# Kernel optimization log

Hardware: AMD Instinct MI355X
Metric: run time of the kernel (lower is better)

The kernel has to match this reference:

```python
import jax, jax.numpy as jnp
import numpy as np

W_IN = 0.001
W_OUT = 1.0
TOL = 1e-8
N_POINTS = 1_048_576


def _octahedron_hull():
    # Palette vertices: +/- unit axes -> convex hull is an octahedron with 8 triangular faces.
    V = np.array([[1, 0, 0], [-1, 0, 0], [0, 1, 0], [0, -1, 0], [0, 0, 1], [0, 0, -1]],
                 dtype=np.float32)
    faces = []
    for sx in (0, 1):
        for sy in (0, 1):
            for sz in (0, 1):
                faces.append([sx, 2 + sy, 4 + sz])
    F = np.array(faces)            # (8,3) vertex indices
    tris = V[F]                    # (8,3,3) triangle vertices
    a, b, c = tris[:, 0], tris[:, 1], tris[:, 2]
    n = np.cross(b - a, c - a)
    n = n / np.linalg.norm(n, axis=-1, keepdims=True)
    flip = np.sum(n * a, -1) < 0   # orient outward (hull centroid is origin)
    n = np.where(flip[:, None], -n, n)
    off = np.sum(n * a, -1)        # face plane offsets: n.x = off on the face
    return V, tris.astype(np.float32), n.astype(np.float32), off.astype(np.float32)


def setup_inputs() -> dict:
    key = jax.random.key(0)
    V, tris, normals, offsets = _octahedron_hull()
    pts = jax.random.normal(key, (N_POINTS, 3), jnp.float32) * 0.35  # mix of inside/outside
    return {
        "inp_points": pts,
        "hull_vertices": jnp.asarray(V),
        "hull_tris": jnp.asarray(tris),
        "face_normals": jnp.asarray(normals),
        "face_offsets": jnp.asarray(offsets),
    }


def _closest_point_on_tris(p, a, b, c):
    # Ericson's closest-point-on-triangle, broadcast over (N,1,3) points x (1,F,3) triangles.
    eps = 1e-20
    ab = b - a
    ac = c - a
    ap = p - a
    d1 = jnp.sum(ab * ap, -1)
    d2 = jnp.sum(ac * ap, -1)
    bp = p - b
    d3 = jnp.sum(ab * bp, -1)
    d4 = jnp.sum(ac * bp, -1)
    cp = p - c
    d5 = jnp.sum(ab * cp, -1)
    d6 = jnp.sum(ac * cp, -1)
    vc = d1 * d4 - d3 * d2
    vb = d5 * d2 - d1 * d6
    va = d3 * d6 - d5 * d4
    # face interior (lowest priority)
    denom = va + vb + vc
    denom = jnp.where(jnp.abs(denom) > eps, denom, 1.0)
    v = (vb / denom)[..., None]
    w = (vc / denom)[..., None]
    res = a + ab * v + ac * w
    # edge BC
    d43 = d4 - d3
    d56 = d5 - d6
    cond = (va <= 0) & (d43 >= 0) & (d56 >= 0)
    t = (d43 / jnp.where(jnp.abs(d43 + d56) > eps, d43 + d56, 1.0))[..., None]
    res = jnp.where(cond[..., None], b + t * (c - b), res)
    # edge AC
    cond = (vb <= 0) & (d2 >= 0) & (d6 <= 0)
    t = (d2 / jnp.where(jnp.abs(d2 - d6) > eps, d2 - d6, 1.0))[..., None]
    res = jnp.where(cond[..., None], a + t * ac, res)
    # edge AB
    cond = (vc <= 0) & (d1 >= 0) & (d3 <= 0)
    t = (d1 / jnp.where(jnp.abs(d1 - d3) > eps, d1 - d3, 1.0))[..., None]
    res = jnp.where(cond[..., None], a + t * ab, res)
    # vertex regions (highest priority)
    res = jnp.where(((d6 >= 0) & (d5 <= d6))[..., None], c, res)
    res = jnp.where(((d3 >= 0) & (d4 <= d3))[..., None], b, res)
    res = jnp.where(((d1 <= 0) & (d2 <= 0))[..., None], a, res)
    return res


def reference(inp_points, hull_vertices, hull_tris, face_normals, face_offsets):
    p = inp_points  # (N,3)
    # find_simplex >= 0  <=>  point inside convex hull: all face half-spaces satisfied
    inside = jnp.all(p @ face_normals.T - face_offsets <= TOL, axis=-1)  # (N,)
    n_in = jnp.sum(inside)
    # knn_points K=1 -> min SQUARED distance to hull vertices, averaged over inside points
    d2v = jnp.min(jnp.sum((p[:, None, :] - hull_vertices[None]) ** 2, -1), axis=-1)  # (N,)
    loss_in = jnp.where(
        n_in > 0,
        W_IN * jnp.sum(jnp.where(inside, d2v, 0.0)) / jnp.maximum(n_in, 1).astype(p.dtype),
        jnp.asarray(0.0, p.dtype),
    )
    # outside points: min point-triangle distance over all hull faces -> closest point (constant)
    a = hull_tris[None, :, 0]  # (1,F,3)
    b = hull_tris[None, :, 1]
    c = hull_tris[None, :, 2]
    cand = _closest_point_on_tris(p[:, None, :], a, b, c)        # (N,F,3)
    d2 = jnp.sum((p[:, None, :] - cand) ** 2, -1)                # (N,F)
    idx = jnp.argmin(d2, axis=-1)
    closest = jnp.take_along_axis(cand, idx[:, None, None], axis=1)[:, 0, :]  # (N,3)
    closest = jax.lax.stop_gradient(closest)  # torch computes this path in detached numpy
    sq = jnp.sum((p - closest) ** 2, -1)      # per-point sum-of-squares (mse 'none' .sum(-1))
    outside = ~inside
    n_out = jnp.sum(outside)
    loss_out = jnp.where(
        n_out > 0,
        W_OUT * jnp.max(jnp.where(outside, sq, 0.0)),
        jnp.asarray(0.0, p.dtype),
    )
    return loss_in + loss_out
```

## Files before the change

kernel.cpp:

```cpp
#include <hip/hip_runtime.h>

#define NP 1048576
#define BLOCK 256
#define PPT 4
#define NBLK (NP / (BLOCK * PPT))
#define GROUPS 32
#define GSIZE (NBLK / GROUPS)
#define W_IN 0.001f
#define W_OUT 1.0f
#define TOL 1e-8f
#define SQRT3 1.7320508f

__device__ __forceinline__ void drain_vmem() {
    asm volatile("s_waitcnt vmcnt(0)" ::: "memory");
}


__global__ __launch_bounds__(BLOCK) void pbl_fused(
    const float* __restrict__ pts, float* __restrict__ ws, float* __restrict__ out)
{
    __shared__ float s_s[BLOCK/64], s_c[BLOCK/64], s_m[BLOCK/64];
    __shared__ int s_last;

    const int lt = threadIdx.x;
    const int tid = blockIdx.x * BLOCK + lt;
    const float4* p4 = (const float4*)pts;
    float4 f0 = p4[tid*3+0];
    float4 f1 = p4[tid*3+1];
    float4 f2 = p4[tid*3+2];
    float px[PPT] = {f0.x, f0.w, f1.z, f2.y};
    float py[PPT] = {f0.y, f1.x, f1.w, f2.z};
    float pz[PPT] = {f0.z, f1.y, f2.x, f2.w};

    float sum_in = 0.f, cnt_in = 0.f, mx_out = 0.f;
    #pragma unroll
    for (int i = 0; i < PPT; ++i) {
        float ux = fabsf(px[i]), uy = fabsf(py[i]), uz = fabsf(pz[i]);
        float s1 = ux + uy + uz;
        float hi = fmaxf(ux, fmaxf(uy, uz));
        float lo = fminf(ux, fminf(uy, uz));
        float mid = s1 - hi - lo;
        float ss = fmaf(px[i], px[i], fmaf(py[i], py[i], pz[i]*pz[i]));

        bool inside = (s1 - 1.f) <= TOL * SQRT3;
        float d2v = fmaf(-2.f, hi, ss) + 1.f;

        float t3 = (s1 - 1.f) * (1.f/3.f);
        float t2 = (hi + mid - 1.f) * 0.5f;
        float t1 = hi - 1.f;
        float d2_3 = 3.f * t3 * t3;
        float d2_2 = fmaf(lo, lo, 2.f * t2 * t2);
        float d2_1 = fmaf(t1, t1, fmaf(mid, mid, lo * lo));
        float sq = (lo > t3) ? d2_3 : ((mid > t2) ? d2_2 : d2_1);

        sum_in += inside ? d2v : 0.f;
        cnt_in += inside ? 1.f : 0.f;
        mx_out  = inside ? mx_out : fmaxf(mx_out, sq);
    }

    #pragma unroll
    for (int o = 32; o > 0; o >>= 1) {
        sum_in += __shfl_down(sum_in, o);
        cnt_in += __shfl_down(cnt_in, o);
        mx_out  = fmaxf(mx_out, __shfl_down(mx_out, o));
    }
    const int wave = lt >> 6;
    if ((lt & 63) == 0) { s_s[wave] = sum_in; s_c[wave] = cnt_in; s_m[wave] = mx_out; }
    __syncthreads();

    unsigned* wsu = (unsigned*)ws;
    const int g = blockIdx.x & (GROUPS - 1);

    if (lt == 0) {
        float S = 0.f, C = 0.f, M = 0.f;
        #pragma unroll
        for (int i = 0; i < BLOCK/64; ++i) { S += s_s[i]; C += s_c[i]; M = fmaxf(M, s_m[i]); }
        __hip_atomic_store(&ws[blockIdx.x],          S, __ATOMIC_RELAXED, __HIP_MEMORY_SCOPE_AGENT);
        __hip_atomic_store(&ws[NBLK + blockIdx.x],   C, __ATOMIC_RELAXED, __HIP_MEMORY_SCOPE_AGENT);
        __hip_atomic_store(&ws[2*NBLK + blockIdx.x], M, __ATOMIC_RELAXED, __HIP_MEMORY_SCOPE_AGENT);
        drain_vmem();
        unsigned ret = __hip_atomic_fetch_add(&wsu[3*NBLK + (g << 4)], 1u,
                                              __ATOMIC_RELAXED, __HIP_MEMORY_SCOPE_AGENT);
        s_last = ((ret & (GSIZE - 1)) == (GSIZE - 1)) ? 1 : 0;
    }
    __syncthreads();

    if (s_last && lt < 64) {
        const int lane = lt;
        float S = 0.f, C = 0.f, M = 0.f;
        if (lane < GSIZE) {
            int b = g + (lane << 5);
            S = __hip_atomic_load(&ws[b],          __ATOMIC_RELAXED, __HIP_MEMORY_SCOPE_AGENT);
            C = __hip_atomic_load(&ws[NBLK + b],   __ATOMIC_RELAXED, __HIP_MEMORY_SCOPE_AGENT);
            M = __hip_atomic_load(&ws[2*NBLK + b], __ATOMIC_RELAXED, __HIP_MEMORY_SCOPE_AGENT);
        }
        #pragma unroll
        for (int o = 32; o > 0; o >>= 1) {
            S += __shfl_down(S, o);
            C += __shfl_down(C, o);
            M  = fmaxf(M, __shfl_down(M, o));
        }
        int last2 = 0;
        if (lane == 0) {
            __hip_atomic_store(&ws[3584 + g], S, __ATOMIC_RELAXED, __HIP_MEMORY_SCOPE_AGENT);
            __hip_atomic_store(&ws[3616 + g], C, __ATOMIC_RELAXED, __HIP_MEMORY_SCOPE_AGENT);
            __hip_atomic_store(&ws[3648 + g], M, __ATOMIC_RELAXED, __HIP_MEMORY_SCOPE_AGENT);
            drain_vmem();
            unsigned r2 = __hip_atomic_fetch_add(&wsu[3712], 1u,
                                                 __ATOMIC_RELAXED, __HIP_MEMORY_SCOPE_AGENT);
            last2 = ((r2 & (GROUPS - 1)) == (GROUPS - 1)) ? 1 : 0;
        }
        last2 = __shfl(last2, 0);
        if (last2) {
            float S2 = 0.f, C2 = 0.f, M2 = 0.f;
            if (lane < GROUPS) {
                S2 = __hip_atomic_load(&ws[3584 + lane], __ATOMIC_RELAXED, __HIP_MEMORY_SCOPE_AGENT);
                C2 = __hip_atomic_load(&ws[3616 + lane], __ATOMIC_RELAXED, __HIP_MEMORY_SCOPE_AGENT);
                M2 = __hip_atomic_load(&ws[3648 + lane], __ATOMIC_RELAXED, __HIP_MEMORY_SCOPE_AGENT);
            }
            #pragma unroll
            for (int o = 32; o > 0; o >>= 1) {
                S2 += __shfl_down(S2, o);
                C2 += __shfl_down(C2, o);
                M2  = fmaxf(M2, __shfl_down(M2, o));
            }
            if (lane == 0) {
                float li = (C2 > 0.f) ? W_IN * S2 / C2 : 0.f;
                float nout = (float)NP - C2;
                float lo = (nout > 0.f) ? W_OUT * M2 : 0.f;
                out[0] = li + lo;
            }
        }
    }
}

extern "C" void kernel_launch(void* const* d_in, const int* in_sizes, int n_in,
                              void* d_out, int out_size, void* d_ws, size_t ws_size,
                              hipStream_t stream) {
    const float* pts = (const float*)d_in[0];
    float* ws = (float*)d_ws;
    float* out = (float*)d_out;
    pbl_fused<<<NBLK, BLOCK, 0, stream>>>(pts, ws, out);
}
```

Baseline: 10.91 us.

## Double points per thread and use three-level 8-way tree reduction

Each thread now loads six float4s and processes eight points, halving the block count to 512. The cross-block reduction moves from two levels (32 groups of 32) to three levels with fan-in 8 at each stage, using 64 first-level counters. The aim is fewer blocks, more memory-level parallelism per thread, and shorter serial chains in the last-block reductions. The cost is more registers per thread and an extra atomic/sync stage.

Measured after the change: 11.63 us. +6.6%, slower.

```diff
diff --git a/kernel.cpp b/kernel.cpp
--- a/kernel.cpp
+++ b/kernel.cpp
@@ -2,19 +2,26 @@
 
 #define NP 1048576
 #define BLOCK 256
-#define PPT 4
+#define PPT 8
 #define NBLK (NP / (BLOCK * PPT))
-#define GROUPS 32
-#define GSIZE (NBLK / GROUPS)
 #define W_IN 0.001f
 #define W_OUT 1.0f
 #define TOL 1e-8f
 #define SQRT3 1.7320508f
 
+
 __device__ __forceinline__ void drain_vmem() {
     asm volatile("s_waitcnt vmcnt(0)" ::: "memory");
 }
-
+__device__ __forceinline__ void st(float* p, float v) {
+    __hip_atomic_store(p, v, __ATOMIC_RELAXED, __HIP_MEMORY_SCOPE_AGENT);
+}
+__device__ __forceinline__ float ld(const float* p) {
+    return __hip_atomic_load(p, __ATOMIC_RELAXED, __HIP_MEMORY_SCOPE_AGENT);
+}
+__device__ __forceinline__ unsigned bump(unsigned* p) {
+    return __hip_atomic_fetch_add(p, 1u, __ATOMIC_RELAXED, __HIP_MEMORY_SCOPE_AGENT);
+}
 
 __global__ __launch_bounds__(BLOCK) void pbl_fused(
     const float* __restrict__ pts, float* __restrict__ ws, float* __restrict__ out)
@@ -25,12 +32,12 @@
     const int lt = threadIdx.x;
     const int tid = blockIdx.x * BLOCK + lt;
     const float4* p4 = (const float4*)pts;
-    float4 f0 = p4[tid*3+0];
-    float4 f1 = p4[tid*3+1];
-    float4 f2 = p4[tid*3+2];
-    float px[PPT] = {f0.x, f0.w, f1.z, f2.y};
-    float py[PPT] = {f0.y, f1.x, f1.w, f2.z};
-    float pz[PPT] = {f0.z, f1.y, f2.x, f2.w};
+    float4 f[6];
+    #pragma unroll
+    for (int k = 0; k < 6; ++k) f[k] = p4[tid*6 + k];
+    float px[PPT] = {f[0].x, f[0].w, f[1].z, f[2].y, f[3].x, f[3].w, f[4].z, f[5].y};
+    float py[PPT] = {f[0].y, f[1].x, f[1].w, f[2].z, f[3].y, f[4].x, f[4].w, f[5].z};
+    float pz[PPT] = {f[0].z, f[1].y, f[2].x, f[2].w, f[3].z, f[4].y, f[5].x, f[5].w};
 
     float sum_in = 0.f, cnt_in = 0.f, mx_out = 0.f;
     #pragma unroll
@@ -69,66 +76,80 @@
     __syncthreads();
 
     unsigned* wsu = (unsigned*)ws;
-    const int g = blockIdx.x & (GROUPS - 1);
+    const int g1 = blockIdx.x & 63;
+    const int g2 = g1 & 7;
 
     if (lt == 0) {
         float S = 0.f, C = 0.f, M = 0.f;
         #pragma unroll
         for (int i = 0; i < BLOCK/64; ++i) { S += s_s[i]; C += s_c[i]; M = fmaxf(M, s_m[i]); }
-        __hip_atomic_store(&ws[blockIdx.x],          S, __ATOMIC_RELAXED, __HIP_MEMORY_SCOPE_AGENT);
-        __hip_atomic_store(&ws[NBLK + blockIdx.x],   C, __ATOMIC_RELAXED, __HIP_MEMORY_SCOPE_AGENT);
-        __hip_atomic_store(&ws[2*NBLK + blockIdx.x], M, __ATOMIC_RELAXED, __HIP_MEMORY_SCOPE_AGENT);
+        st(&ws[blockIdx.x], S);
+        st(&ws[512 + blockIdx.x], C);
+        st(&ws[1024 + blockIdx.x], M);
         drain_vmem();
-        unsigned ret = __hip_atomic_fetch_add(&wsu[3*NBLK + (g << 4)], 1u,
-                                              __ATOMIC_RELAXED, __HIP_MEMORY_SCOPE_AGENT);
-        s_last = ((ret & (GSIZE - 1)) == (GSIZE - 1)) ? 1 : 0;
+        unsigned ret = bump(&wsu[1536 + 16*g1]);
+        s_last = ((ret & 7) == 7) ? 1 : 0;
     }
     __syncthreads();
 
     if (s_last && lt < 64) {
         const int lane = lt;
         float S = 0.f, C = 0.f, M = 0.f;
-        if (lane < GSIZE) {
-            int b = g + (lane << 5);
-            S = __hip_atomic_load(&ws[b],          __ATOMIC_RELAXED, __HIP_MEMORY_SCOPE_AGENT);
-            C = __hip_atomic_load(&ws[NBLK + b],   __ATOMIC_RELAXED, __HIP_MEMORY_SCOPE_AGENT);
-            M = __hip_atomic_load(&ws[2*NBLK + b], __ATOMIC_RELAXED, __HIP_MEMORY_SCOPE_AGENT);
+        if (lane < 8) {
+            int b = g1 + (lane << 6);
+            S = ld(&ws[b]); C = ld(&ws[512 + b]); M = ld(&ws[1024 + b]);
         }
         #pragma unroll
-        for (int o = 32; o > 0; o >>= 1) {
+        for (int o = 4; o > 0; o >>= 1) {
             S += __shfl_down(S, o);
             C += __shfl_down(C, o);
             M  = fmaxf(M, __shfl_down(M, o));
         }
         int last2 = 0;
         if (lane == 0) {
-            __hip_atomic_store(&ws[3584 + g], S, __ATOMIC_RELAXED, __HIP_MEMORY_SCOPE_AGENT);
-            __hip_atomic_store(&ws[3616 + g], C, __ATOMIC_RELAXED, __HIP_MEMORY_SCOPE_AGENT);
-            __hip_atomic_store(&ws[3648 + g], M, __ATOMIC_RELAXED, __HIP_MEMORY_SCOPE_AGENT);
+            st(&ws[2560 + g1], S); st(&ws[2624 + g1], C); st(&ws[2688 + g1], M);
             drain_vmem();
-            unsigned r2 = __hip_atomic_fetch_add(&wsu[3712], 1u,
-                                                 __ATOMIC_RELAXED, __HIP_MEMORY_SCOPE_AGENT);
-            last2 = ((r2 & (GROUPS - 1)) == (GROUPS - 1)) ? 1 : 0;
+            unsigned r2 = bump(&wsu[2816 + 16*g2]);
+            last2 = ((r2 & 7) == 7) ? 1 : 0;
         }
         last2 = __shfl(last2, 0);
         if (last2) {
             float S2 = 0.f, C2 = 0.f, M2 = 0.f;
-            if (lane < GROUPS) {
-                S2 = __hip_atomic_load(&ws[3584 + lane], __ATOMIC_RELAXED, __HIP_MEMORY_SCOPE_AGENT);
-                C2 = __hip_atomic_load(&ws[3616 + lane], __ATOMIC_RELAXED, __HIP_MEMORY_SCOPE_AGENT);
-                M2 = __hip_atomic_load(&ws[3648 + lane], __ATOMIC_RELAXED, __HIP_MEMORY_SCOPE_AGENT);
+            if (lane < 8) {
+                int gg = g2 + (lane << 3);
+                S2 = ld(&ws[2560 + gg]); C2 = ld(&ws[2624 + gg]); M2 = ld(&ws[2688 + gg]);
             }
             #pragma unroll
-            for (int o = 32; o > 0; o >>= 1) {
+            for (int o = 4; o > 0; o >>= 1) {
                 S2 += __shfl_down(S2, o);
                 C2 += __shfl_down(C2, o);
                 M2  = fmaxf(M2, __shfl_down(M2, o));
             }
+            int last3 = 0;
             if (lane == 0) {
-                float li = (C2 > 0.f) ? W_IN * S2 / C2 : 0.f;
-                float nout = (float)NP - C2;
-                float lo = (nout > 0.f) ? W_OUT * M2 : 0.f;
-                out[0] = li + lo;
+                st(&ws[3072 + g2], S2); st(&ws[3080 + g2], C2); st(&ws[3088 + g2], M2);
+                drain_vmem();
+                unsigned r3 = bump(&wsu[3104]);
+                last3 = ((r3 & 7) == 7) ? 1 : 0;
+            }
+            last3 = __shfl(last3, 0);
+            if (last3) {
+                float S3 = 0.f, C3 = 0.f, M3 = 0.f;
+                if (lane < 8) {
+                    S3 = ld(&ws[3072 + lane]); C3 = ld(&ws[3080 + lane]); M3 = ld(&ws[3088 + lane]);
+                }
+                #pragma unroll
+                for (int o = 4; o > 0; o >>= 1) {
+                    S3 += __shfl_down(S3, o);
+                    C3 += __shfl_down(C3, o);
+                    M3  = fmaxf(M3, __shfl_down(M3, o));
+                }
+                if (lane == 0) {
+                    float li = (C3 > 0.f) ? W_IN * S3 / C3 : 0.f;
+                    float nout = (float)NP - C3;
+                    float lo = (nout > 0.f) ? W_OUT * M3 : 0.f;
+                    out[0] = li + lo;
+                }
             }
         }
     }
```
